# Optimization experiments

Hardware: AMD Instinct MI355X
Metric: run time of the kernel (lower is better)

Reference implementation:

```python
import jax, jax.numpy as jnp
import numpy as np

HEADS = 8
RANK = 4

def _lora(x, w_down, w_up, palette, in_dim, out_dim):
    # w_down: [RANK*in_dim, 15], w_up: [RANK*out_dim, 15], palette: [1, 15]
    down = (palette @ w_down.T).reshape(RANK, in_dim)   # [r, in]
    up = (palette @ w_up.T).reshape(out_dim, RANK)      # [out, r]
    return (x @ down.T) @ up.T                          # [..., out]


def setup_inputs() -> dict:
    key = jax.random.key(0)
    ks = jax.random.split(key, 16)
    B, S, D = 2, 2048, 1280
    def n(k, shape, std=0.02):
        return (jax.random.normal(k, shape, dtype=jnp.float32) * std).astype(jnp.float32)
    return {
        'hidden_states': jax.random.normal(ks[0], (B, S, D), dtype=jnp.float32),
        'color_palette': jax.random.uniform(ks[1], (1, 15), dtype=jnp.float32),
        'Wq': n(ks[2], (D, D)), 'Wk': n(ks[3], (D, D)),
        'Wv': n(ks[4], (D, D)), 'Wo': n(ks[5], (D, D)),
        'bo': jnp.zeros((D,), dtype=jnp.float32),
        'q_down': n(ks[6], (RANK * D, 15), 0.25), 'q_up': n(ks[7], (RANK * D, 15)),
        'k_down': n(ks[8], (RANK * D, 15), 0.25), 'k_up': n(ks[9], (RANK * D, 15)),
        'v_down': n(ks[10], (RANK * D, 15), 0.25), 'v_up': n(ks[11], (RANK * D, 15)),
        'o_down': n(ks[12], (RANK * D, 15), 0.25), 'o_up': n(ks[13], (RANK * D, 15)),
    }


def reference(hidden_states, color_palette, Wq, Wk, Wv, Wo, bo,
              q_down, q_up, k_down, k_up, v_down, v_up, o_down, o_up):
    B, S, D = hidden_states.shape
    H = HEADS
    hd = D // H
    scale = 1.0  # LoRA scale
    x = hidden_states
    # LoRA-augmented projections (self-attention: encoder_hidden_states = x)
    q = x @ Wq.T + scale * _lora(x, q_down, q_up, color_palette, D, D)
    k = x @ Wk.T + scale * _lora(x, k_down, k_up, color_palette, D, D)
    v = x @ Wv.T + scale * _lora(x, v_down, v_up, color_palette, D, D)
    # split heads: [B, S, D] -> [B, H, S, hd]
    q = q.reshape(B, S, H, hd).transpose(0, 2, 1, 3)
    k = k.reshape(B, S, H, hd).transpose(0, 2, 1, 3)
    v = v.reshape(B, S, H, hd).transpose(0, 2, 1, 3)
    attn_scale = 1.0 / jnp.sqrt(jnp.asarray(hd, dtype=q.dtype))
    scores = jnp.einsum('bhqd,bhkd->bhqk', q, k) * attn_scale
    probs = jax.nn.softmax(scores, axis=-1)
    out = jnp.einsum('bhqk,bhkd->bhqd', probs, v)
    out = out.transpose(0, 2, 1, 3).reshape(B, S, D)
    out = out @ Wo.T + bo + scale * _lora(out, o_down, o_up, color_palette, D, D)
    return out
```

## Files before the change

kernel.cpp:

```cpp
#include <hip/hip_runtime.h>

typedef unsigned short u16;
typedef unsigned int u32;
typedef __attribute__((ext_vector_type(4))) float floatx4;
typedef __attribute__((ext_vector_type(8))) __bf16 bf16x8;

#define MFMA_BF16(a, b, c) __builtin_amdgcn_mfma_f32_16x16x32_bf16((a), (b), (c), 0, 0, 0)

typedef const __attribute__((address_space(1))) void* gas_ptr;
typedef __attribute__((address_space(3))) void* las_ptr;

__device__ __forceinline__ void gll16(const void* g, void* l) {
  __builtin_amdgcn_global_load_lds((gas_ptr)g, (las_ptr)l, 16, 0, 0);
}

__device__ __forceinline__ u16 f2bf(float x) {
  u32 u = __builtin_bit_cast(u32, x);
  u = (u + 0x7fffu + ((u >> 16) & 1u)) >> 16;
  return (u16)u;
}

__global__ void prep_downup(const float* __restrict__ pal,
                            const float* __restrict__ qd, const float* __restrict__ qu,
                            const float* __restrict__ kd, const float* __restrict__ ku,
                            const float* __restrict__ vd, const float* __restrict__ vu,
                            const float* __restrict__ od, const float* __restrict__ ou,
                            float* __restrict__ down_f, float* __restrict__ up_f) {
  int tid = blockIdx.x * blockDim.x + threadIdx.x;
  int w = tid / 10240;
  int rem = tid - w * 10240;
  const float* dsrc = (w == 0) ? qd : (w == 1) ? kd : (w == 2) ? vd : od;
  const float* usrc = (w == 0) ? qu : (w == 1) ? ku : (w == 2) ? vu : ou;
  bool isdown = rem < 5120;
  int row = isdown ? rem : rem - 5120;
  const float* src = (isdown ? dsrc : usrc) + row * 15;
  float s = 0.f;
#pragma unroll
  for (int p = 0; p < 15; ++p) s += pal[p] * src[p];
  if (isdown) down_f[w * 5120 + row] = s;
  else        up_f[w * 5120 + row] = s;
}

__global__ void build_weff(const float* __restrict__ Wq, const float* __restrict__ Wk,
                           const float* __restrict__ Wv, const float* __restrict__ Wo,
                           const float* __restrict__ down_f, const float* __restrict__ up_f,
                           u16* __restrict__ weff_qkv, u16* __restrict__ weff_o) {
  int tid = blockIdx.x * blockDim.x + threadIdx.x;
  int w = tid / 1638400;
  int rem = tid - w * 1638400;
  int n = rem / 1280;
  int k = rem - n * 1280;
  const float* W = (w == 0) ? Wq : (w == 1) ? Wk : (w == 2) ? Wv : Wo;
  const float* up = up_f + w * 5120 + n * 4;
  const float* dn = down_f + w * 5120 + k;
  float v = W[rem] + up[0] * dn[0] + up[1] * dn[1280] + up[2] * dn[2560] + up[3] * dn[3840];
  u16 hv = f2bf(v);
  if (w < 3) weff_qkv[w * 1638400 + rem] = hv;
  else       weff_o[rem] = hv;
}

__global__ void cvt_x(const float4* __restrict__ x, ushort4* __restrict__ xb) {
  int i = blockIdx.x * blockDim.x + threadIdx.x;
  float4 v = x[i];
  ushort4 o;
  o.x = f2bf(v.x); o.y = f2bf(v.y); o.z = f2bf(v.z); o.w = f2bf(v.w);
  xb[i] = o;
}

__global__ __launch_bounds__(256) void gemm128_qkv(const u16* __restrict__ A, const u16* __restrict__ Bm,
                                                   u16* __restrict__ qb, u16* __restrict__ kb,
                                                   u16* __restrict__ vbuf, int K) {
  __shared__ __align__(16) u16 lA[128 * 64];
  __shared__ __align__(16) u16 lB[128 * 64];
  const int t = threadIdx.x;
  const int lane = t & 63;
  const int l15 = lane & 15, quad = lane >> 4;
  const int wid = t >> 6;
  const int wm = (wid >> 1) * 64;
  const int wn = (wid & 1) * 64;
  const int bm = blockIdx.x * 128;
  const int bn = blockIdx.y * 128;
  floatx4 acc[4][4] = {};

  int soff[4];
#pragma unroll
  for (int i = 0; i < 4; ++i) {
    int c = t + i * 256;
    int row = c >> 3, pos = c & 7;
    soff[i] = row * K + ((pos + row) & 7) * 8;
  }
  int afo[4][2], bfo[4][2];
#pragma unroll
  for (int i = 0; i < 4; ++i) {
#pragma unroll
    for (int ch = 0; ch < 2; ++ch) {
      int ra = wm + i * 16 + l15;
      int rb = wn + i * 16 + l15;
      int kc8 = ch * 4 + quad;
      afo[i][ch] = ra * 64 + ((kc8 - ra) & 7) * 8;
      bfo[i][ch] = rb * 64 + ((kc8 - rb) & 7) * 8;
    }
  }

  const u16* Ab = A + (long)bm * K;
  const u16* Bb = Bm + (long)bn * K;
  const int nkt = K >> 6;

  for (int kt = 0; kt < nkt; ++kt) {
    __syncthreads();
    const int k0 = kt * 64;
#pragma unroll
    for (int i = 0; i < 4; ++i) gll16(Ab + (long)soff[i] + k0, lA + (t + i * 256) * 8);
#pragma unroll
    for (int i = 0; i < 4; ++i) gll16(Bb + (long)soff[i] + k0, lB + (t + i * 256) * 8);
    __syncthreads();
#pragma unroll
    for (int ch = 0; ch < 2; ++ch) {
      bf16x8 af[4], bfr[4];
#pragma unroll
      for (int i = 0; i < 4; ++i) af[i] = *(const bf16x8*)(lA + afo[i][ch]);
#pragma unroll
      for (int i = 0; i < 4; ++i) bfr[i] = *(const bf16x8*)(lB + bfo[i][ch]);
#pragma unroll
      for (int i = 0; i < 4; ++i)
#pragma unroll
        for (int j = 0; j < 4; ++j)
          acc[i][j] = MFMA_BF16(af[i], bfr[j], acc[i][j]);
    }
  }

#pragma unroll
  for (int i = 0; i < 4; ++i) {
#pragma unroll
    for (int j = 0; j < 4; ++j) {
#pragma unroll
      for (int r = 0; r < 4; ++r) {
        int m = bm + wm + i * 16 + quad * 4 + r;
        int n = bn + wn + j * 16 + l15;
        u16 hv = f2bf(acc[i][j][r]);
        if (n < 1280) {
          qb[(long)m * 1280 + n] = hv;
        } else if (n < 2560) {
          kb[(long)m * 1280 + (n - 1280)] = hv;
        } else {
          vbuf[(long)m * 1280 + (n - 2560)] = hv;
        }
      }
    }
  }
}

__global__ __launch_bounds__(256) void vtrans(const u16* __restrict__ vbuf,
                                              u16* __restrict__ vtb) {
  __shared__ u16 tile[64 * 65];
  const int t = threadIdx.x;
  const int sb = blockIdx.x * 64, nb = blockIdx.y * 64, b = blockIdx.z;
  const u16* src = vbuf + ((long)(b * 2048 + sb)) * 1280 + nb;
#pragma unroll
  for (int it = 0; it < 16; ++it) {
    int idx = t + it * 256;
    int s = idx >> 6, n = idx & 63;
    tile[s * 65 + n] = src[(long)s * 1280 + n];
  }
  __syncthreads();
  u16* dst = vtb + ((long)(b * 1280 + nb)) * 2048 + sb;
#pragma unroll
  for (int it = 0; it < 16; ++it) {
    int idx = t + it * 256;
    int n = idx >> 6, s = idx & 63;
    dst[(long)n * 2048 + s] = tile[s * 65 + n];
  }
}

__global__ __launch_bounds__(256) void gemm64_o(const u16* __restrict__ A, const u16* __restrict__ Bm,
                                                float* __restrict__ outf,
                                                const float* __restrict__ bias, int K) {
  __shared__ __align__(16) u16 lA[64 * 64];
  __shared__ __align__(16) u16 lB[128 * 64];
  const int t = threadIdx.x;
  const int lane = t & 63;
  const int l15 = lane & 15, quad = lane >> 4;
  const int wid = t >> 6;
  const int bm = blockIdx.x * 64;
  const int bn = blockIdx.y * 128;
  floatx4 acc[4][2] = {};

  int aoff[2], boff[4];
#pragma unroll
  for (int i = 0; i < 2; ++i) {
    int c = t + i * 256;
    int row = c >> 3, pos = c & 7;
    aoff[i] = row * K + ((pos + row) & 7) * 8;
  }
#pragma unroll
  for (int i = 0; i < 4; ++i) {
    int c = t + i * 256;
    int row = c >> 3, pos = c & 7;
    boff[i] = row * K + ((pos + row) & 7) * 8;
  }
  int afo[4][2], bfo[2][2];
#pragma unroll
  for (int ch = 0; ch < 2; ++ch) {
    int kc8 = ch * 4 + quad;
#pragma unroll
    for (int i = 0; i < 4; ++i) {
      int ra = i * 16 + l15;
      afo[i][ch] = ra * 64 + ((kc8 - ra) & 7) * 8;
    }
#pragma unroll
    for (int j = 0; j < 2; ++j) {
      int rb = wid * 32 + j * 16 + l15;
      bfo[j][ch] = rb * 64 + ((kc8 - rb) & 7) * 8;
    }
  }

  const u16* Ab = A + (long)bm * K;
  const u16* Bb = Bm + (long)bn * K;
  const int nkt = K >> 6;

  for (int kt = 0; kt < nkt; ++kt) {
    __syncthreads();
    const int k0 = kt * 64;
#pragma unroll
    for (int i = 0; i < 2; ++i) gll16(Ab + (long)aoff[i] + k0, lA + (t + i * 256) * 8);
#pragma unroll
    for (int i = 0; i < 4; ++i) gll16(Bb + (long)boff[i] + k0, lB + (t + i * 256) * 8);
    __syncthreads();
#pragma unroll
    for (int ch = 0; ch < 2; ++ch) {
      bf16x8 af[4], bfr[2];
#pragma unroll
      for (int i = 0; i < 4; ++i) af[i] = *(const bf16x8*)(lA + afo[i][ch]);
#pragma unroll
      for (int j = 0; j < 2; ++j) bfr[j] = *(const bf16x8*)(lB + bfo[j][ch]);
#pragma unroll
      for (int i = 0; i < 4; ++i)
#pragma unroll
        for (int j = 0; j < 2; ++j)
          acc[i][j] = MFMA_BF16(af[i], bfr[j], acc[i][j]);
    }
  }

#pragma unroll
  for (int i = 0; i < 4; ++i) {
#pragma unroll
    for (int j = 0; j < 2; ++j) {
#pragma unroll
      for (int r = 0; r < 4; ++r) {
        int m = bm + i * 16 + quad * 4 + r;
        int n = bn + wid * 32 + j * 16 + l15;
        outf[(long)m * 1280 + n] = acc[i][j][r] + bias[n];
      }
    }
  }
}

__global__ __launch_bounds__(256) void flash_attn(const u16* __restrict__ qb,
                                                  const u16* __restrict__ kb,
                                                  const u16* __restrict__ vtb,
                                                  u16* __restrict__ attn) {
  const int S = 2048, D = 1280, HD = 160;
  __shared__ __align__(16) u16 kt_lds[64 * 160];
  __shared__ __align__(16) u16 vt_lds[160 * 64];
  __shared__ __align__(16) u16 p_lds[4][16 * 76];
  const int t = threadIdx.x, lane = t & 63, wid = t >> 6;
  const int quad = lane >> 4, l15 = lane & 15;
  const int bh = blockIdx.y, b = bh >> 3, h = bh & 7;
  const int q0 = blockIdx.x * 64 + wid * 16;
  const float kS = 0.11404582025f;

  bf16x8 aq[5];
  {
    const u16* qg = qb + ((long)(b * 2048 + q0 + l15)) * D + h * HD + quad * 8;
#pragma unroll
    for (int dc = 0; dc < 5; ++dc) aq[dc] = *(const bf16x8*)(qg + dc * 32);
  }

  const u16* kg[5];
  const u16* vg[5];
  {
    const u16* kgbase = kb + ((long)(b * 2048)) * D + h * HD;
    const u16* vgbase = vtb + ((long)(b * 1280 + h * HD)) * 2048;
#pragma unroll
    for (int i = 0; i < 5; ++i) {
      int c = t + i * 256;
      int key = c / 20, rot = c - key * 20;
      int ccol = rot - (key % 20);
      if (ccol < 0) ccol += 20;
      kg[i] = kgbase + (long)key * D + ccol * 8;
      int vrow = c >> 3, swz = c & 7;
      int vcol = swz ^ (vrow & 7);
      vg[i] = vgbase + (long)vrow * 2048 + vcol * 8;
    }
  }

  int kfo[4][5];
#pragma unroll
  for (int j = 0; j < 4; ++j) {
    int key = j * 16 + l15;
    int r0 = (quad + key) % 20;
#pragma unroll
    for (int dc = 0; dc < 5; ++dc) {
      int rot = r0 + dc * 4;
      if (rot >= 20) rot -= 20;
      kfo[j][dc] = (key * 20 + rot) * 8;
    }
  }
  int vfo[10][2];
#pragma unroll
  for (int dc = 0; dc < 10; ++dc) {
    int row = dc * 16 + l15;
#pragma unroll
    for (int ks = 0; ks < 2; ++ks) {
      int sw = (ks * 4 + quad) ^ (row & 7);
      vfo[dc][ks] = (row * 8 + sw) * 8;
    }
  }

  float l_part[4] = {0.f, 0.f, 0.f, 0.f};
  floatx4 o_acc[10] = {};

  for (int kt0 = 0; kt0 < S; kt0 += 64) {
    __syncthreads();
#pragma unroll
    for (int i = 0; i < 5; ++i) gll16(kg[i], kt_lds + (t + i * 256) * 8);
#pragma unroll
    for (int i = 0; i < 5; ++i) gll16(vg[i], vt_lds + (t + i * 256) * 8);
#pragma unroll
    for (int i = 0; i < 5; ++i) { kg[i] += (long)64 * D; vg[i] += 64; }
    __syncthreads();

    floatx4 s[4] = {};
#pragma unroll
    for (int dc = 0; dc < 5; ++dc) {
#pragma unroll
      for (int j = 0; j < 4; ++j) {
        bf16x8 kf = *(const bf16x8*)(kt_lds + kfo[j][dc]);
        s[j] = MFMA_BF16(aq[dc], kf, s[j]);
      }
    }

#pragma unroll
    for (int r = 0; r < 4; ++r) {
      float p0 = __builtin_exp2f(fminf(s[0][r] * kS, 80.f));
      float p1 = __builtin_exp2f(fminf(s[1][r] * kS, 80.f));
      float p2 = __builtin_exp2f(fminf(s[2][r] * kS, 80.f));
      float p3 = __builtin_exp2f(fminf(s[3][r] * kS, 80.f));
      l_part[r] += (p0 + p1) + (p2 + p3);
      u16* pw = p_lds[wid] + (quad * 4 + r) * 76 + l15;
      pw[0]  = f2bf(p0);
      pw[16] = f2bf(p1);
      pw[32] = f2bf(p2);
      pw[48] = f2bf(p3);
    }
    asm volatile("s_waitcnt lgkmcnt(0)" ::: "memory");

    bf16x8 paA = *(const bf16x8*)(p_lds[wid] + l15 * 76 + quad * 8);
    bf16x8 paB = *(const bf16x8*)(p_lds[wid] + l15 * 76 + 32 + quad * 8);
#pragma unroll
    for (int dc = 0; dc < 10; ++dc) {
      bf16x8 vfA = *(const bf16x8*)(vt_lds + vfo[dc][0]);
      bf16x8 vfB = *(const bf16x8*)(vt_lds + vfo[dc][1]);
      o_acc[dc] = MFMA_BF16(paA, vfA, o_acc[dc]);
      o_acc[dc] = MFMA_BF16(paB, vfB, o_acc[dc]);
    }
  }

  float rl[4];
#pragma unroll
  for (int r = 0; r < 4; ++r) {
    float rs = l_part[r];
    rs += __shfl_xor(rs, 1, 64);
    rs += __shfl_xor(rs, 2, 64);
    rs += __shfl_xor(rs, 4, 64);
    rs += __shfl_xor(rs, 8, 64);
    rl[r] = 1.0f / rs;
  }
#pragma unroll
  for (int dc = 0; dc < 10; ++dc) {
#pragma unroll
    for (int r = 0; r < 4; ++r) {
      float v = o_acc[dc][r] * rl[r];
      int row = q0 + quad * 4 + r;
      int col = h * HD + dc * 16 + l15;
      attn[((long)(b * 2048 + row)) * D + col] = f2bf(v);
    }
  }
}

extern "C" void kernel_launch(void* const* d_in, const int* in_sizes, int n_in,
                              void* d_out, int out_size, void* d_ws, size_t ws_size,
                              hipStream_t stream) {
  const float* x   = (const float*)d_in[0];
  const float* pal = (const float*)d_in[1];
  const float* Wq  = (const float*)d_in[2];
  const float* Wk  = (const float*)d_in[3];
  const float* Wv  = (const float*)d_in[4];
  const float* Wo  = (const float*)d_in[5];
  const float* bo  = (const float*)d_in[6];
  const float* qd  = (const float*)d_in[7];
  const float* qu  = (const float*)d_in[8];
  const float* kd  = (const float*)d_in[9];
  const float* ku  = (const float*)d_in[10];
  const float* vd  = (const float*)d_in[11];
  const float* vu  = (const float*)d_in[12];
  const float* od  = (const float*)d_in[13];
  const float* ou  = (const float*)d_in[14];
  float* out = (float*)d_out;

  char* ws = (char*)d_ws;
  u16* xb       = (u16*)(ws);
  u16* weff_qkv = (u16*)(ws + 10485760);
  u16* weff_o   = (u16*)(ws + 20316160);
  u16* qbuf     = (u16*)(ws + 23592960);
  u16* kbuf     = (u16*)(ws + 34078720);
  u16* vtb      = (u16*)(ws + 44564480);
  u16* attn     = (u16*)(ws + 55050240);
  float* down_f = (float*)(ws + 65536000);
  float* up_f   = (float*)(ws + 65617920);
  u16* vbuf     = (u16*)(ws + 65699840);

  prep_downup<<<160, 256, 0, stream>>>(pal, qd, qu, kd, ku, vd, vu, od, ou, down_f, up_f);
  build_weff<<<25600, 256, 0, stream>>>(Wq, Wk, Wv, Wo, down_f, up_f, weff_qkv, weff_o);
  cvt_x<<<5120, 256, 0, stream>>>((const float4*)x, (ushort4*)xb);
  gemm128_qkv<<<dim3(32, 30), 256, 0, stream>>>(xb, weff_qkv, qbuf, kbuf, vbuf, 1280);
  vtrans<<<dim3(32, 20, 2), 256, 0, stream>>>(vbuf, vtb);
  flash_attn<<<dim3(32, 16), 256, 0, stream>>>(qbuf, kbuf, vtb, attn);
  gemm64_o<<<dim3(64, 10), 256, 0, stream>>>(attn, weff_o, out, bo, 1280);
}
```

Before: 301.8 us.

## Switch flash attention to 32x32 MFMA with key-split warps and LDS merge

The attention kernel now uses 32x32x16 bf16 MFMA instead of 16x16x32. Each warp handles a 32-query subtile over half of each 64-key tile, so the four warps form two query groups times two key halves. At the end, one key half writes its partial output and row sums to shared memory and the other half combines them before writing the result. The larger MFMA shape is meant to cut LDS fragment reads per FLOP and improve matrix-unit efficiency. In exchange it adds a final shared-memory merge step and rounds one partial output to bf16 before the sum.

After: 338.8 us. 12.3% more time.

```diff
diff --git a/kernel.cpp b/kernel.cpp
--- a/kernel.cpp
+++ b/kernel.cpp
@@ -3,9 +3,11 @@
 typedef unsigned short u16;
 typedef unsigned int u32;
 typedef __attribute__((ext_vector_type(4))) float floatx4;
+typedef __attribute__((ext_vector_type(16))) float floatx16;
 typedef __attribute__((ext_vector_type(8))) __bf16 bf16x8;
 
 #define MFMA_BF16(a, b, c) __builtin_amdgcn_mfma_f32_16x16x32_bf16((a), (b), (c), 0, 0, 0)
+#define MFMA32_BF16(a, b, c) __builtin_amdgcn_mfma_f32_32x32x16_bf16((a), (b), (c), 0, 0, 0)
 
 typedef const __attribute__((address_space(1))) void* gas_ptr;
 typedef __attribute__((address_space(3))) void* las_ptr;
@@ -260,20 +262,23 @@
                                                   const u16* __restrict__ vtb,
                                                   u16* __restrict__ attn) {
   const int S = 2048, D = 1280, HD = 160;
-  __shared__ __align__(16) u16 kt_lds[64 * 160];
-  __shared__ __align__(16) u16 vt_lds[160 * 64];
-  __shared__ __align__(16) u16 p_lds[4][16 * 76];
+  __shared__ __align__(16) u16 sh[25600];
+  __shared__ float l_sh[64];
+  u16* kt_lds = sh;
+  u16* vt_lds = sh + 10240;
   const int t = threadIdx.x, lane = t & 63, wid = t >> 6;
-  const int quad = lane >> 4, l15 = lane & 15;
+  const int l31 = lane & 31, half = lane >> 5;
   const int bh = blockIdx.y, b = bh >> 3, h = bh & 7;
-  const int q0 = blockIdx.x * 64 + wid * 16;
+  const int qsub = wid & 1, kh = wid >> 1;
+  const int q0 = blockIdx.x * 64 + qsub * 32;
   const float kS = 0.11404582025f;
-
-  bf16x8 aq[5];
+  u16* p_my = sh + 20480 + wid * 1280;
+
+  bf16x8 aq[10];
   {
-    const u16* qg = qb + ((long)(b * 2048 + q0 + l15)) * D + h * HD + quad * 8;
-#pragma unroll
-    for (int dc = 0; dc < 5; ++dc) aq[dc] = *(const bf16x8*)(qg + dc * 32);
+    const u16* qg = qb + ((long)(b * 2048 + q0 + l31)) * D + h * HD + half * 8;
+#pragma unroll
+    for (int dc = 0; dc < 10; ++dc) aq[dc] = *(const bf16x8*)(qg + dc * 16);
   }
 
   const u16* kg[5];
@@ -294,31 +299,32 @@
     }
   }
 
-  int kfo[4][5];
-#pragma unroll
-  for (int j = 0; j < 4; ++j) {
-    int key = j * 16 + l15;
-    int r0 = (quad + key) % 20;
-#pragma unroll
-    for (int dc = 0; dc < 5; ++dc) {
-      int rot = r0 + dc * 4;
-      if (rot >= 20) rot -= 20;
-      kfo[j][dc] = (key * 20 + rot) * 8;
-    }
-  }
-  int vfo[10][2];
-#pragma unroll
-  for (int dc = 0; dc < 10; ++dc) {
-    int row = dc * 16 + l15;
-#pragma unroll
-    for (int ks = 0; ks < 2; ++ks) {
-      int sw = (ks * 4 + quad) ^ (row & 7);
-      vfo[dc][ks] = (row * 8 + sw) * 8;
-    }
-  }
-
-  float l_part[4] = {0.f, 0.f, 0.f, 0.f};
-  floatx4 o_acc[10] = {};
+  int kfo[10];
+  {
+    int keyrow = kh * 32 + l31;
+#pragma unroll
+    for (int dc = 0; dc < 10; ++dc) {
+      int c20 = dc * 2 + half;
+      int pos = c20 + keyrow % 20;
+      pos = (c20 + keyrow) % 20;
+      kfo[dc] = (keyrow * 20 + pos) * 8;
+    }
+  }
+  int vfo[5][2];
+#pragma unroll
+  for (int ng = 0; ng < 5; ++ng) {
+    int row = ng * 32 + l31;
+#pragma unroll
+    for (int kc = 0; kc < 2; ++kc) {
+      int sw = (kh * 4 + kc * 2 + half) ^ (row & 7);
+      vfo[ng][kc] = (row * 8 + sw) * 8;
+    }
+  }
+
+  float l_part[16];
+#pragma unroll
+  for (int r = 0; r < 16; ++r) l_part[r] = 0.f;
+  floatx16 o_acc[5] = {};
 
   for (int kt0 = 0; kt0 < S; kt0 += 64) {
     __syncthreads();
@@ -330,60 +336,71 @@
     for (int i = 0; i < 5; ++i) { kg[i] += (long)64 * D; vg[i] += 64; }
     __syncthreads();
 
-    floatx4 s[4] = {};
-#pragma unroll
-    for (int dc = 0; dc < 5; ++dc) {
-#pragma unroll
-      for (int j = 0; j < 4; ++j) {
-        bf16x8 kf = *(const bf16x8*)(kt_lds + kfo[j][dc]);
-        s[j] = MFMA_BF16(aq[dc], kf, s[j]);
-      }
-    }
-
-#pragma unroll
-    for (int r = 0; r < 4; ++r) {
-      float p0 = __builtin_exp2f(fminf(s[0][r] * kS, 80.f));
-      float p1 = __builtin_exp2f(fminf(s[1][r] * kS, 80.f));
-      float p2 = __builtin_exp2f(fminf(s[2][r] * kS, 80.f));
-      float p3 = __builtin_exp2f(fminf(s[3][r] * kS, 80.f));
-      l_part[r] += (p0 + p1) + (p2 + p3);
-      u16* pw = p_lds[wid] + (quad * 4 + r) * 76 + l15;
-      pw[0]  = f2bf(p0);
-      pw[16] = f2bf(p1);
-      pw[32] = f2bf(p2);
-      pw[48] = f2bf(p3);
+    floatx16 s = {};
+#pragma unroll
+    for (int dc = 0; dc < 10; ++dc) {
+      bf16x8 kf = *(const bf16x8*)(kt_lds + kfo[dc]);
+      s = MFMA32_BF16(aq[dc], kf, s);
+    }
+
+#pragma unroll
+    for (int reg = 0; reg < 16; ++reg) {
+      int row = (reg & 3) + 8 * (reg >> 2) + 4 * half;
+      float p = __builtin_exp2f(fminf(s[reg] * kS, 80.f));
+      l_part[reg] += p;
+      p_my[row * 40 + l31] = f2bf(p);
     }
     asm volatile("s_waitcnt lgkmcnt(0)" ::: "memory");
 
-    bf16x8 paA = *(const bf16x8*)(p_lds[wid] + l15 * 76 + quad * 8);
-    bf16x8 paB = *(const bf16x8*)(p_lds[wid] + l15 * 76 + 32 + quad * 8);
-#pragma unroll
-    for (int dc = 0; dc < 10; ++dc) {
-      bf16x8 vfA = *(const bf16x8*)(vt_lds + vfo[dc][0]);
-      bf16x8 vfB = *(const bf16x8*)(vt_lds + vfo[dc][1]);
-      o_acc[dc] = MFMA_BF16(paA, vfA, o_acc[dc]);
-      o_acc[dc] = MFMA_BF16(paB, vfB, o_acc[dc]);
-    }
-  }
-
-  float rl[4];
-#pragma unroll
-  for (int r = 0; r < 4; ++r) {
-    float rs = l_part[r];
+    bf16x8 pa0 = *(const bf16x8*)(p_my + l31 * 40 + half * 8);
+    bf16x8 pa1 = *(const bf16x8*)(p_my + l31 * 40 + 16 + half * 8);
+#pragma unroll
+    for (int ng = 0; ng < 5; ++ng) {
+      bf16x8 vf0 = *(const bf16x8*)(vt_lds + vfo[ng][0]);
+      bf16x8 vf1 = *(const bf16x8*)(vt_lds + vfo[ng][1]);
+      o_acc[ng] = MFMA32_BF16(pa0, vf0, o_acc[ng]);
+      o_acc[ng] = MFMA32_BF16(pa1, vf1, o_acc[ng]);
+    }
+  }
+
+  float l_red[16];
+#pragma unroll
+  for (int reg = 0; reg < 16; ++reg) {
+    float rs = l_part[reg];
     rs += __shfl_xor(rs, 1, 64);
     rs += __shfl_xor(rs, 2, 64);
     rs += __shfl_xor(rs, 4, 64);
     rs += __shfl_xor(rs, 8, 64);
-    rl[r] = 1.0f / rs;
-  }
-#pragma unroll
-  for (int dc = 0; dc < 10; ++dc) {
-#pragma unroll
-    for (int r = 0; r < 4; ++r) {
-      float v = o_acc[dc][r] * rl[r];
-      int row = q0 + quad * 4 + r;
-      int col = h * HD + dc * 16 + l15;
-      attn[((long)(b * 2048 + row)) * D + col] = f2bf(v);
+    rs += __shfl_xor(rs, 16, 64);
+    l_red[reg] = rs;
+  }
+
+  __syncthreads();
+  if (kh == 1) {
+#pragma unroll
+    for (int reg = 0; reg < 16; ++reg) {
+      int row = (reg & 3) + 8 * (reg >> 2) + 4 * half;
+      int rl = qsub * 32 + row;
+      if (l31 == 0) l_sh[rl] = l_red[reg];
+#pragma unroll
+      for (int ng = 0; ng < 5; ++ng)
+        sh[rl * 168 + ng * 32 + l31] = f2bf(o_acc[ng][reg]);
+    }
+  }
+  __syncthreads();
+  if (kh == 0) {
+#pragma unroll
+    for (int reg = 0; reg < 16; ++reg) {
+      int row = (reg & 3) + 8 * (reg >> 2) + 4 * half;
+      int rl = qsub * 32 + row;
+      float inv = 1.0f / (l_red[reg] + l_sh[rl]);
+      long grow = (long)(b * 2048 + blockIdx.x * 64 + rl);
+#pragma unroll
+      for (int ng = 0; ng < 5; ++ng) {
+        float other = (float)__builtin_bit_cast(__bf16, sh[rl * 168 + ng * 32 + l31]);
+        float v = (o_acc[ng][reg] + other) * inv;
+        attn[grow * D + h * HD + ng * 32 + l31] = f2bf(v);
+      }
     }
   }
 }
```
